# Optimization experiments

Hardware: AMD Instinct MI355X
Metric: run time of the kernel (lower is better)

Reference implementation:

```python
import jax, jax.numpy as jnp
import numpy as np

TEMP = 0.025
BN_EPS = 1e-5


def _attention(a, W_in, b_in, g, beta, rm, rv, W_out, b_out):
    # a: (b, n1, n2, P, Q); 1x1 conv over the Q 'channel' dim, gate, softmax over P.
    m = a.mean(axis=3)                                   # (b,n1,n2,Q)
    t = jnp.einsum('bnmq,kq->bnmk', m, W_in) + b_in      # (b,n1,n2,K)
    t = jax.nn.relu((t - rm) / jnp.sqrt(rv + BN_EPS) * g + beta)
    t = jnp.einsum('bnmk,qk->bnmq', t, W_out) + b_out    # (b,n1,n2,Q)
    s = jnp.mean(a * t[:, :, :, None, :], axis=-1)       # (b,n1,n2,P)
    return jax.nn.softmax(s / TEMP, axis=-1) + 1.0


def _cam_forward(zf, xf, conv1_w, conv1_b, bn1_g, bn1_b, bn1_rm, bn1_rv,
                 conv2_w, conv2_b, conv3_w, conv3_b, bn3_g, bn3_b, bn3_rm, bn3_rv,
                 conv4_w, conv4_b):
    out1, out2 = [], []
    L = zf.shape[0]
    for l in range(L):  # small fixed loop over feature levels
        f1, f2 = zf[l], xf[l]
        b, c, h1, w1 = f1.shape
        h2, w2 = f2.shape[2], f2.shape[3]
        P, Q = h1 * w1, h2 * w2
        f1s = jnp.stack([f1.reshape(b, c, P)] * 2, axis=1)   # (b,2,c,P)
        f2s = jnp.stack([f2.reshape(b, c, Q)] * 2, axis=1)   # (b,2,c,Q)
        f1n = f1s / jnp.maximum(jnp.linalg.norm(f1s, axis=2, keepdims=True), 1e-12)
        f2n = f2s / jnp.maximum(jnp.linalg.norm(f2s, axis=2, keepdims=True), 1e-12)
        a1 = jnp.einsum('bncp,bmcq->bnmpq', f1n, f2n)        # (b,2,2,P,Q)
        att1 = _attention(a1, conv1_w, conv1_b, bn1_g, bn1_b, bn1_rm, bn1_rv,
                          conv2_w, conv2_b)                  # (b,2,2,P)
        att2 = _attention(a1.swapaxes(3, 4), conv3_w, conv3_b, bn3_g, bn3_b,
                          bn3_rm, bn3_rv, conv4_w, conv4_b)  # (b,2,2,Q)
        # mean over the (n1,n2)=(2,2) pair grid without materializing (b,2,2,c,HW)
        o1 = jnp.einsum('bncp,bnmp->bcp', f1s, att1) / 4.0
        o2 = jnp.einsum('bmcq,bnmq->bcq', f2s, att2) / 4.0
        out1.append(o1.reshape(b, c, h1, w1))
        out2.append(o2.reshape(b, c, h2, w2))
    return (jnp.stack(out1), jnp.stack(out2))


def setup_inputs() -> dict:
    key = jax.random.key(0)
    ks = jax.random.split(key, 12)
    L, B, C = 3, 32, 256
    inp = {
        'zf': jax.random.normal(ks[0], (L, B, C, 7, 7), jnp.float32),
        'xf': jax.random.normal(ks[1], (L, B, C, 31, 31), jnp.float32),
        'conv1_w': jax.random.normal(ks[2], (31, 961), jnp.float32) * np.sqrt(2.0 / 31),
        'conv1_b': jax.random.normal(ks[3], (31,), jnp.float32) * 0.05,
        'bn1_g': jax.random.uniform(ks[4], (31,), jnp.float32, 0.5, 1.5),
        'bn1_b': jax.random.normal(ks[5], (31,), jnp.float32) * 0.05,
        'bn1_rm': jnp.zeros((31,), jnp.float32),
        'bn1_rv': jnp.ones((31,), jnp.float32),
        'conv2_w': jax.random.normal(ks[6], (961, 31), jnp.float32) * np.sqrt(2.0 / 961),
        'conv2_b': jax.random.normal(ks[7], (961,), jnp.float32) * 0.05,
        'conv3_w': jax.random.normal(ks[8], (7, 49), jnp.float32) * np.sqrt(2.0 / 7),
        'conv3_b': jax.random.normal(ks[9], (7,), jnp.float32) * 0.05,
        'bn3_g': jax.random.uniform(ks[10], (7,), jnp.float32, 0.5, 1.5),
        'bn3_b': jax.random.normal(ks[11], (7,), jnp.float32) * 0.05,
        'bn3_rm': jnp.zeros((7,), jnp.float32),
        'bn3_rv': jnp.ones((7,), jnp.float32),
        'conv4_w': jax.random.normal(jax.random.fold_in(key, 100), (49, 7), jnp.float32) * np.sqrt(2.0 / 49),
        'conv4_b': jax.random.normal(jax.random.fold_in(key, 101), (49,), jnp.float32) * 0.05,
    }
    return inp


def reference(zf, xf, conv1_w, conv1_b, bn1_g, bn1_b, bn1_rm, bn1_rv,
              conv2_w, conv2_b, conv3_w, conv3_b, bn3_g, bn3_b, bn3_rm, bn3_rv,
              conv4_w, conv4_b):
    return _cam_forward(zf, xf, conv1_w, conv1_b, bn1_g, bn1_b, bn1_rm, bn1_rv,
                        conv2_w, conv2_b, conv3_w, conv3_b, bn3_g, bn3_b,
                        bn3_rm, bn3_rv, conv4_w, conv4_b)
```

## Files before the change

kernel.cpp:

```cpp
#include <hip/hip_runtime.h>
#include <math.h>

#define NLB 96
#define CC  256
#define PP  49
#define QQ  961
#define QP  1024
#define TEMP_INV 40.0f
#define BN_EPS 1e-5f

#define N1 (NLB*CC*PP)
#define N2 (NLB*CC*QQ)

__global__ __launch_bounds__(256) void prep_z(
    const float* __restrict__ zf, float* __restrict__ inv1_ws,
    float* __restrict__ w_ws)
{
    const int lb = blockIdx.x;
    const int tid = threadIdx.x;
    __shared__ float f1L[CC * PP];
    __shared__ float inv1L[PP];
    const float* __restrict__ f1 = zf + (size_t)lb * CC * PP;
    for (int i = tid; i < CC * PP; i += 256) f1L[i] = f1[i];
    __syncthreads();
    if (tid < PP) {
        float ss = 0.f;
        for (int c = 0; c < CC; ++c) { const float x = f1L[c * PP + tid]; ss = fmaf(x, x, ss); }
        const float iv = 1.0f / fmaxf(sqrtf(ss), 1e-12f);
        inv1L[tid] = iv;
        inv1_ws[lb * 64 + tid] = iv;
    }
    __syncthreads();
    {
        float s = 0.f;
#pragma unroll
        for (int p = 0; p < PP; ++p) s = fmaf(inv1L[p], f1L[tid * PP + p], s);
        w_ws[lb * CC + tid] = s;
    }
}

__global__ __launch_bounds__(256) void xpass1(
    const float* __restrict__ xf, const float* __restrict__ w_ws,
    float* __restrict__ ssp, float* __restrict__ dcp)
{
    const int qg = blockIdx.x;
    const int ch = blockIdx.y;
    const int lb = blockIdx.z;
    const int tid = threadIdx.x;
    const int q  = qg * 256 + tid;
    const bool qv = (q < QQ);
    const int qc = qv ? q : QQ - 1;

    __shared__ float wL[128];
    if (tid < 128) wL[tid] = w_ws[lb * CC + ch * 128 + tid];
    __syncthreads();

    const float* __restrict__ base =
        xf + (size_t)lb * CC * QQ + (size_t)(ch * 128) * QQ + qc;

    float ss = 0.f, dc = 0.f;
    for (int c0 = 0; c0 < 128; c0 += 16) {
        float x[16];
#pragma unroll
        for (int j = 0; j < 16; ++j) x[j] = base[(size_t)(c0 + j) * QQ];
#pragma unroll
        for (int j = 0; j < 16; ++j) {
            ss = fmaf(x[j], x[j], ss);
            dc = fmaf(wL[c0 + j], x[j], dc);
        }
    }
    if (qv) {
        ssp[((size_t)ch * NLB + lb) * QP + q] = ss;
        dcp[((size_t)ch * NLB + lb) * QP + q] = dc;
    }
}

__global__ __launch_bounds__(1024) void finq_kernel(
    const float* __restrict__ ssp, const float* __restrict__ dcp,
    float* __restrict__ inv2_ws, float* __restrict__ mcol_ws)
{
    const int lb = blockIdx.x;
    const int q = threadIdx.x;
    if (q >= QQ) return;
    const float ss = ssp[((size_t)0 * NLB + lb) * QP + q] +
                     ssp[((size_t)1 * NLB + lb) * QP + q];
    const float dc = dcp[((size_t)0 * NLB + lb) * QP + q] +
                     dcp[((size_t)1 * NLB + lb) * QP + q];
    const float iv2 = 1.0f / fmaxf(sqrtf(ss), 1e-12f);
    inv2_ws[lb * QP + q] = iv2;
    mcol_ws[lb * QP + q] = dc * iv2 * (1.0f / PP);
}

__global__ __launch_bounds__(512) void vpass_kernel(
    const float* __restrict__ xf, const float* __restrict__ wq_ws,
    float* __restrict__ vout_ws)
{
    const int cb = blockIdx.x;
    const int lb = blockIdx.y;
    const int tid  = threadIdx.x;
    const int lane = tid & 63;
    const int wave = tid >> 6;

    __shared__ float wqL[QP];
    for (int i = tid; i < QP; i += 512)
        wqL[i] = (i < QQ) ? wq_ws[lb * QP + i] : 0.f;
    __syncthreads();

    const float* __restrict__ f2 = xf + (size_t)lb * CC * QQ;

#pragma unroll
    for (int r = 0; r < 8; ++r) {
        const int c = cb * 64 + wave * 8 + r;
        const float* __restrict__ row = f2 + (size_t)c * QQ;
        float x[16];
#pragma unroll
        for (int j = 0; j < 16; ++j) {
            const int qi = j * 64 + lane;
            x[j] = row[qi < QQ ? qi : QQ - 1];
        }
        float s = 0.f;
#pragma unroll
        for (int j = 0; j < 16; ++j) s = fmaf(x[j], wqL[j * 64 + lane], s);
        for (int off = 32; off > 0; off >>= 1) s += __shfl_xor(s, off, 64);
        if (lane == 0) vout_ws[lb * CC + c] = s;
    }
}

__global__ __launch_bounds__(512) void mid_kernel(
    const float* __restrict__ zf, const float* __restrict__ v_ws,
    const float* __restrict__ inv1_ws, const float* __restrict__ mcol_ws,
    const float* __restrict__ inv2_ws,
    const float* __restrict__ W1, const float* __restrict__ b1,
    const float* __restrict__ g1, const float* __restrict__ bb1,
    const float* __restrict__ rm1, const float* __restrict__ rv1,
    const float* __restrict__ W2, const float* __restrict__ b2,
    const float* __restrict__ W3, const float* __restrict__ b3,
    const float* __restrict__ g3, const float* __restrict__ bb3,
    const float* __restrict__ rm3, const float* __restrict__ rv3,
    const float* __restrict__ W4, const float* __restrict__ b4,
    float* __restrict__ wgt_ws, float* __restrict__ wb_ws)
{
    const int lb = blockIdx.x;
    const int tid = threadIdx.x;
    __shared__ float f1L[CC * PP];
    __shared__ float inv1L[64], vL[CC], mrowL[PP];
    __shared__ float mcolL[QQ];
    __shared__ float taL[31], tbL[7], t2bL[PP];

    const float* __restrict__ f1 = zf + (size_t)lb * CC * PP;
    for (int i = tid; i < CC * PP; i += 512) f1L[i] = f1[i];
    if (tid < 64) inv1L[tid] = inv1_ws[lb * 64 + tid];
    if (tid >= 64 && tid < 64 + CC) vL[tid - 64] = v_ws[lb * CC + tid - 64];
    for (int q = tid; q < QQ; q += 512) mcolL[q] = mcol_ws[lb * QP + q];
    __syncthreads();

    if (tid < PP) {
        float s = 0.f;
        for (int c = 0; c < CC; ++c) s = fmaf(f1L[c * PP + tid], vL[c], s);
        mrowL[tid] = s * inv1L[tid] * (1.0f / QQ);
    }
    if (tid < 31 * 16) {
        const int k = tid >> 4, sub = tid & 15;
        float s = 0.f;
        for (int q = sub; q < QQ; q += 16) s = fmaf(mcolL[q], W1[k * QQ + q], s);
        s += __shfl_xor(s, 1, 64); s += __shfl_xor(s, 2, 64);
        s += __shfl_xor(s, 4, 64); s += __shfl_xor(s, 8, 64);
        if (sub == 0) {
            float t = s + b1[k];
            t = (t - rm1[k]) * rsqrtf(rv1[k] + BN_EPS) * g1[k] + bb1[k];
            taL[k] = fmaxf(t, 0.f);
        }
    }
    __syncthreads();
    if (tid < 7 * 8) {
        const int k = tid >> 3, sub = tid & 7;
        float s = 0.f;
        for (int p = sub; p < PP; p += 8) s = fmaf(mrowL[p], W3[k * PP + p], s);
        s += __shfl_xor(s, 1, 64); s += __shfl_xor(s, 2, 64); s += __shfl_xor(s, 4, 64);
        if (sub == 0) {
            float t = s + b3[k];
            t = (t - rm3[k]) * rsqrtf(rv3[k] + BN_EPS) * g3[k] + bb3[k];
            tbL[k] = fmaxf(t, 0.f);
        }
    }
    __syncthreads();
    if (tid < PP) {
        float s = b4[tid];
#pragma unroll
        for (int k = 0; k < 7; ++k) s = fmaf(tbL[k], W4[tid * 7 + k], s);
        t2bL[tid] = s;
    }
    for (int q = tid; q < QQ; q += 512) {
        float s = b2[q];
#pragma unroll
        for (int k = 0; k < 31; ++k) s = fmaf(taL[k], W2[q * 31 + k], s);
        wgt_ws[lb * QP + q] = s * inv2_ws[lb * QP + q];
    }
    __syncthreads();
    if (tid < CC) {
        float s = 0.f;
#pragma unroll
        for (int p = 0; p < PP; ++p) s = fmaf(inv1L[p] * t2bL[p], f1L[tid * PP + p], s);
        wb_ws[lb * CC + tid] = s;
    }
}

__global__ __launch_bounds__(256) void xpass2(
    const float* __restrict__ xf, const float* __restrict__ wb_ws,
    float* __restrict__ s2p)
{
    const int qg = blockIdx.x;
    const int ch = blockIdx.y;
    const int lb = blockIdx.z;
    const int tid = threadIdx.x;
    const int q  = qg * 256 + tid;
    const bool qv = (q < QQ);
    const int qc = qv ? q : QQ - 1;

    __shared__ float wbL[128];
    if (tid < 128) wbL[tid] = wb_ws[lb * CC + ch * 128 + tid];
    __syncthreads();

    const float* __restrict__ base =
        xf + (size_t)lb * CC * QQ + (size_t)(ch * 128) * QQ + qc;

    float dwb = 0.f;
    for (int c0 = 0; c0 < 128; c0 += 16) {
        float x[16];
#pragma unroll
        for (int j = 0; j < 16; ++j) x[j] = base[(size_t)(c0 + j) * QQ];
#pragma unroll
        for (int j = 0; j < 16; ++j) dwb = fmaf(wbL[c0 + j], x[j], dwb);
    }
    if (qv) s2p[((size_t)ch * NLB + lb) * QP + q] = dwb;
}

__global__ __launch_bounds__(512) void fin_kernel(
    const float* __restrict__ zf, const float* __restrict__ vb_ws,
    const float* __restrict__ inv1_ws, const float* __restrict__ s2p,
    const float* __restrict__ inv2_ws,
    float* __restrict__ att1_ws, float* __restrict__ att2_ws)
{
    const int lb = blockIdx.x;
    const int tid = threadIdx.x;
    const int lane = tid & 63;
    const int wv = tid >> 6;
    __shared__ float f1L[CC * PP];
    __shared__ float vbL[CC], inv1L[64], s1L[PP];
    __shared__ float s2L[QQ];
    __shared__ float redM[8], redS[8];

    const float* __restrict__ f1 = zf + (size_t)lb * CC * PP;
    for (int i = tid; i < CC * PP; i += 512) f1L[i] = f1[i];
    if (tid < CC) vbL[tid] = vb_ws[lb * CC + tid];
    if (tid >= 256 && tid < 320) inv1L[tid - 256] = inv1_ws[lb * 64 + tid - 256];
    for (int q = tid; q < QQ; q += 512)
        s2L[q] = (s2p[((size_t)0 * NLB + lb) * QP + q] +
                  s2p[((size_t)1 * NLB + lb) * QP + q]) *
                 inv2_ws[lb * QP + q] * (1.0f / PP) * TEMP_INV;
    __syncthreads();

    if (tid < PP) {
        float s = 0.f;
        for (int c = 0; c < CC; ++c) s = fmaf(f1L[c * PP + tid], vbL[c], s);
        s1L[tid] = s * inv1L[tid] * (1.0f / QQ) * TEMP_INV;
    }
    __syncthreads();

    if (wv == 0) {
        const float v = (lane < PP) ? s1L[lane] : -3.4e38f;
        float m = v;
        for (int off = 32; off > 0; off >>= 1) m = fmaxf(m, __shfl_xor(m, off, 64));
        const float e = (lane < PP) ? expf(v - m) : 0.f;
        float sum = e;
        for (int off = 32; off > 0; off >>= 1) sum += __shfl_xor(sum, off, 64);
        if (lane < PP) att1_ws[lb * PP + lane] = e / sum + 1.0f;
    }

    float lm = -3.4e38f;
    for (int q = tid; q < QQ; q += 512) lm = fmaxf(lm, s2L[q]);
    for (int off = 32; off > 0; off >>= 1) lm = fmaxf(lm, __shfl_xor(lm, off, 64));
    if (lane == 0) redM[wv] = lm;
    __syncthreads();
    float gm = redM[0];
#pragma unroll
    for (int i = 1; i < 8; ++i) gm = fmaxf(gm, redM[i]);
    float ls = 0.f;
    for (int q = tid; q < QQ; q += 512) ls += expf(s2L[q] - gm);
    for (int off = 32; off > 0; off >>= 1) ls += __shfl_xor(ls, off, 64);
    if (lane == 0) redS[wv] = ls;
    __syncthreads();
    float tot = 0.f;
#pragma unroll
    for (int i = 0; i < 8; ++i) tot += redS[i];
    const float rinv = 1.0f / tot;
    for (int q = tid; q < QQ; q += 512)
        att2_ws[lb * QQ + q] = expf(s2L[q] - gm) * rinv + 1.0f;
}

template <int INNER>
__global__ __launch_bounds__(256) void scale_kernel(
    const float* __restrict__ in, const float* __restrict__ att,
    float* __restrict__ out, int n4)
{
    const int i = blockIdx.x * 256 + threadIdx.x;
    if (i >= n4) return;
    const float4 v = reinterpret_cast<const float4*>(in)[i];
    const float* vv = reinterpret_cast<const float*>(&v);
    float4 o;
    float* ov = reinterpret_cast<float*>(&o);
    const int g = i * 4;
#pragma unroll
    for (int j = 0; j < 4; ++j) {
        const int gg = g + j;
        const int lb = gg / (CC * INNER);
        const int x  = gg % INNER;
        ov[j] = vv[j] * att[lb * INNER + x];
    }
    reinterpret_cast<float4*>(out)[i] = o;
}

extern "C" void kernel_launch(void* const* d_in, const int* in_sizes, int n_in,
                              void* d_out, int out_size, void* d_ws, size_t ws_size,
                              hipStream_t stream)
{
    const float* zf  = (const float*)d_in[0];
    const float* xf  = (const float*)d_in[1];
    const float* W1  = (const float*)d_in[2];
    const float* b1  = (const float*)d_in[3];
    const float* g1  = (const float*)d_in[4];
    const float* bb1 = (const float*)d_in[5];
    const float* rm1 = (const float*)d_in[6];
    const float* rv1 = (const float*)d_in[7];
    const float* W2  = (const float*)d_in[8];
    const float* b2  = (const float*)d_in[9];
    const float* W3  = (const float*)d_in[10];
    const float* b3  = (const float*)d_in[11];
    const float* g3  = (const float*)d_in[12];
    const float* bb3 = (const float*)d_in[13];
    const float* rm3 = (const float*)d_in[14];
    const float* rv3 = (const float*)d_in[15];
    const float* W4  = (const float*)d_in[16];
    const float* b4  = (const float*)d_in[17];

    float* ws = (float*)d_ws;
    float* w    = ws;
    float* v    = w    + (size_t)NLB * CC;
    float* wb   = v    + (size_t)NLB * CC;
    float* vb   = wb   + (size_t)NLB * CC;
    float* inv1 = vb   + (size_t)NLB * CC;
    float* inv2 = inv1 + (size_t)NLB * 64;
    float* mcol = inv2 + (size_t)NLB * QP;
    float* wgt  = mcol + (size_t)NLB * QP;
    float* att1 = wgt  + (size_t)NLB * QP;
    float* att2 = att1 + (size_t)NLB * PP;
    float* ssp  = att2 + (size_t)NLB * QQ;
    float* dcp  = ssp  + (size_t)2 * NLB * QP;
    float* s2p  = dcp  + (size_t)2 * NLB * QP;

    float* out1 = (float*)d_out;
    float* out2 = out1 + N1;

    prep_z<<<NLB, 256, 0, stream>>>(zf, inv1, w);

    dim3 gqs(4, 2, NLB);
    xpass1<<<gqs, 256, 0, stream>>>(xf, w, ssp, dcp);
    finq_kernel<<<NLB, 1024, 0, stream>>>(ssp, dcp, inv2, mcol);

    dim3 gv(4, NLB);
    vpass_kernel<<<gv, 512, 0, stream>>>(xf, inv2, v);

    mid_kernel<<<NLB, 512, 0, stream>>>(zf, v, inv1, mcol, inv2,
        W1, b1, g1, bb1, rm1, rv1, W2, b2,
        W3, b3, g3, bb3, rm3, rv3, W4, b4,
        wgt, wb);

    xpass2<<<gqs, 256, 0, stream>>>(xf, wb, s2p);
    vpass_kernel<<<gv, 512, 0, stream>>>(xf, wgt, vb);

    fin_kernel<<<NLB, 512, 0, stream>>>(zf, vb, inv1, s2p, inv2, att1, att2);

    const int n4_1 = N1 / 4;
    const int n4_2 = N2 / 4;
    scale_kernel<PP><<<(n4_1 + 255) / 256, 256, 0, stream>>>(zf, att1, out1, n4_1);
    scale_kernel<QQ><<<(n4_2 + 255) / 256, 256, 0, stream>>>(xf, att2, out2, n4_2);
}
```

Baseline: 143.6 us.

## Fuse xpass2 and second vpass into one joint pass over xf

Merges the xpass2 kernel (column dot with wb) and the second vpass_kernel (row dot with wgt) into a single kernel that stages 16-row tiles of xf in shared memory and computes both reductions from the same tile. Per-q-group partial sums for vb are written to a new workspace and summed in fin_kernel. This removes one full read of xf (about 94 MB) and one launch, at the cost of extra barriers and wave-level shuffle reductions per tile.

```diff
diff --git a/kernel.cpp b/kernel.cpp
--- a/kernel.cpp
+++ b/kernel.cpp
@@ -205,38 +205,58 @@
     }
 }
 
-__global__ __launch_bounds__(256) void xpass2(
+__global__ __launch_bounds__(256) void xjoint(
     const float* __restrict__ xf, const float* __restrict__ wb_ws,
-    float* __restrict__ s2p)
+    const float* __restrict__ wgt_ws,
+    float* __restrict__ s2p, float* __restrict__ vbp)
 {
     const int qg = blockIdx.x;
     const int ch = blockIdx.y;
     const int lb = blockIdx.z;
-    const int tid = threadIdx.x;
+    const int tid  = threadIdx.x;
+    const int lane = tid & 63;
+    const int wave = tid >> 6;
     const int q  = qg * 256 + tid;
     const bool qv = (q < QQ);
     const int qc = qv ? q : QQ - 1;
 
     __shared__ float wbL[128];
+    __shared__ float wgtL[256];
+    __shared__ __align__(16) float tile[16 * 264];
+
     if (tid < 128) wbL[tid] = wb_ws[lb * CC + ch * 128 + tid];
-    __syncthreads();
+    wgtL[tid] = qv ? wgt_ws[lb * QP + q] : 0.f;
 
     const float* __restrict__ base =
         xf + (size_t)lb * CC * QQ + (size_t)(ch * 128) * QQ + qc;
+    float* __restrict__ vbpo = vbp + ((size_t)(lb * 4 + qg)) * CC + ch * 128;
 
     float dwb = 0.f;
     for (int c0 = 0; c0 < 128; c0 += 16) {
-        float x[16];
-#pragma unroll
-        for (int j = 0; j < 16; ++j) x[j] = base[(size_t)(c0 + j) * QQ];
-#pragma unroll
-        for (int j = 0; j < 16; ++j) dwb = fmaf(wbL[c0 + j], x[j], dwb);
+        __syncthreads();
+#pragma unroll
+        for (int r = 0; r < 16; ++r)
+            tile[r * 264 + tid] = base[(size_t)(c0 + r) * QQ];
+        __syncthreads();
+#pragma unroll
+        for (int r = 0; r < 16; ++r)
+            dwb = fmaf(wbL[c0 + r], tile[r * 264 + tid], dwb);
+#pragma unroll
+        for (int rr = 0; rr < 4; ++rr) {
+            const int r = wave + rr * 4;
+            float s = 0.f;
+#pragma unroll
+            for (int j = 0; j < 4; ++j)
+                s = fmaf(tile[r * 264 + j * 64 + lane], wgtL[j * 64 + lane], s);
+            for (int off = 32; off > 0; off >>= 1) s += __shfl_xor(s, off, 64);
+            if (lane == 0) vbpo[c0 + r] = s;
+        }
     }
     if (qv) s2p[((size_t)ch * NLB + lb) * QP + q] = dwb;
 }
 
 __global__ __launch_bounds__(512) void fin_kernel(
-    const float* __restrict__ zf, const float* __restrict__ vb_ws,
+    const float* __restrict__ zf, const float* __restrict__ vbp,
     const float* __restrict__ inv1_ws, const float* __restrict__ s2p,
     const float* __restrict__ inv2_ws,
     float* __restrict__ att1_ws, float* __restrict__ att2_ws)
@@ -252,7 +272,13 @@
 
     const float* __restrict__ f1 = zf + (size_t)lb * CC * PP;
     for (int i = tid; i < CC * PP; i += 512) f1L[i] = f1[i];
-    if (tid < CC) vbL[tid] = vb_ws[lb * CC + tid];
+    if (tid < CC) {
+        float s = 0.f;
+#pragma unroll
+        for (int qg = 0; qg < 4; ++qg)
+            s += vbp[((size_t)(lb * 4 + qg)) * CC + tid];
+        vbL[tid] = s;
+    }
     if (tid >= 256 && tid < 320) inv1L[tid - 256] = inv1_ws[lb * 64 + tid - 256];
     for (int q = tid; q < QQ; q += 512)
         s2L[q] = (s2p[((size_t)0 * NLB + lb) * QP + q] +
@@ -347,8 +373,7 @@
     float* w    = ws;
     float* v    = w    + (size_t)NLB * CC;
     float* wb   = v    + (size_t)NLB * CC;
-    float* vb   = wb   + (size_t)NLB * CC;
-    float* inv1 = vb   + (size_t)NLB * CC;
+    float* inv1 = wb   + (size_t)NLB * CC;
     float* inv2 = inv1 + (size_t)NLB * 64;
     float* mcol = inv2 + (size_t)NLB * QP;
     float* wgt  = mcol + (size_t)NLB * QP;
@@ -357,6 +382,7 @@
     float* ssp  = att2 + (size_t)NLB * QQ;
     float* dcp  = ssp  + (size_t)2 * NLB * QP;
     float* s2p  = dcp  + (size_t)2 * NLB * QP;
+    float* vbp  = s2p  + (size_t)2 * NLB * QP;
 
     float* out1 = (float*)d_out;
     float* out2 = out1 + N1;
@@ -375,10 +401,9 @@
         W3, b3, g3, bb3, rm3, rv3, W4, b4,
         wgt, wb);
 
-    xpass2<<<gqs, 256, 0, stream>>>(xf, wb, s2p);
-    vpass_kernel<<<gv, 512, 0, stream>>>(xf, wgt, vb);
-
-    fin_kernel<<<NLB, 512, 0, stream>>>(zf, vb, inv1, s2p, inv2, att1, att2);
+    xjoint<<<gqs, 256, 0, stream>>>(xf, wb, wgt, s2p, vbp);
+
+    fin_kernel<<<NLB, 512, 0, stream>>>(zf, vbp, inv1, s2p, inv2, att1, att2);
 
     const int n4_1 = N1 / 4;
     const int n4_2 = N2 / 4;
```

Measured after the change: 133.8 us. -6.8%, faster.
